# Kernel tuning notes

Hardware: AMD Instinct MI355X
Metric: run time of the kernel (lower is better)

Reference implementation:

```python
import jax, jax.numpy as jnp
import numpy as np

N = 100000      # nodes
E = 600000      # edges
IN = 128        # in_dim
HID = 32        # hidden_dim per head (layer 1)
HEADS = 4       # num_heads (layer 1)
NEG_SLOPE = 0.2 # PyG GATConv default negative_slope


def setup_inputs() -> dict:
    key = jax.random.key(0)
    ks = jax.random.split(key, 10)
    x = jax.random.normal(ks[0], (N, IN), dtype=jnp.float32)
    edge_index = jax.random.randint(ks[1], (2, E), 0, N, dtype=jnp.int64)
    # layer 1 params: W1 [IN, HEADS*HID], attention vectors [HEADS, HID], bias [HEADS*HID]
    W1 = jax.random.normal(ks[2], (IN, HEADS * HID), dtype=jnp.float32) / np.float32(np.sqrt(IN))
    att_src1 = jax.random.normal(ks[3], (HEADS, HID), dtype=jnp.float32) * 0.1
    att_dst1 = jax.random.normal(ks[4], (HEADS, HID), dtype=jnp.float32) * 0.1
    b1 = jnp.zeros((HEADS * HID,), dtype=jnp.float32)
    # layer 2 params: heads=1, out channels=1, concat=False
    W2 = jax.random.normal(ks[5], (HEADS * HID, 1), dtype=jnp.float32) / np.float32(np.sqrt(HEADS * HID))
    att_src2 = jax.random.normal(ks[6], (1, 1), dtype=jnp.float32) * 0.1
    att_dst2 = jax.random.normal(ks[7], (1, 1), dtype=jnp.float32) * 0.1
    b2 = jnp.zeros((1,), dtype=jnp.float32)
    return {"x": x, "edge_index": edge_index, "W1": W1, "att_src1": att_src1,
            "att_dst1": att_dst1, "b1": b1, "W2": W2, "att_src2": att_src2,
            "att_dst2": att_dst2, "b2": b2}


def gat_layer(x, src, dst, W, a_src, a_dst, b, heads, ch, concat):
    """PyG GATConv (eval mode): edge score + segment softmax + scatter aggregate."""
    n = x.shape[0]
    h = (x @ W).reshape(n, heads, ch)                    # [N,H,C]
    e_src = jnp.einsum('nhc,hc->nh', h, a_src)           # alpha_src per node
    e_dst = jnp.einsum('nhc,hc->nh', h, a_dst)           # alpha_dst per node
    e = jax.nn.leaky_relu(e_src[src] + e_dst[dst], NEG_SLOPE)  # [E,H]
    m = jax.ops.segment_max(e, dst, num_segments=n)      # stable softmax per dst
    p = jnp.exp(e - m[dst])
    denom = jax.ops.segment_sum(p, dst, num_segments=n)
    alpha = p / (denom[dst] + 1e-16)                     # [E,H]
    out = jax.ops.segment_sum(alpha[:, :, None] * h[src], dst, num_segments=n)  # [N,H,C]
    out = out.reshape(n, heads * ch) if concat else out.mean(axis=1)
    return out + b


def reference(x, edge_index, W1, att_src1, att_dst1, b1, W2, att_src2, att_dst2, b2):
    n = x.shape[0]
    loops = jnp.arange(n, dtype=edge_index.dtype)        # PyG add_self_loops=True
    src = jnp.concatenate([edge_index[0], loops])
    dst = jnp.concatenate([edge_index[1], loops])
    h1 = gat_layer(x, src, dst, W1, att_src1, att_dst1, b1, HEADS, HID, True)   # [N, HEADS*HID]
    out = gat_layer(h1, src, dst, W2, att_src2, att_dst2, b2, 1, 1, False)      # [N, 1]
    return out
```

## Files before the change

### kernel.cpp

```cpp
#include <hip/hip_runtime.h>
#include <hip/hip_fp16.h>
#include <math.h>

#define N_NODES 100000
#define E_EDGES 600000
#define IN_DIM  128
#define HID     32
#define HEADS   4
#define NEG     0.2f
#define CAP     32

typedef __attribute__((ext_vector_type(8))) _Float16 f16x8;
typedef __attribute__((ext_vector_type(4))) float f32x4;

__device__ __forceinline__ float lrelu(float v) { return v > 0.f ? v : NEG * v; }

#define SWZ(r, byteoff) ((byteoff) ^ (((r) & 7) << 4))


__global__ __launch_bounds__(128) void wprep_kernel(const float* __restrict__ W1,
                                                    const float* __restrict__ as1,
                                                    const float* __restrict__ ad1,
                                                    __half* __restrict__ wtx,
                                                    int* __restrict__ cnt) {
    int tid = blockIdx.x * 128 + threadIdx.x;
    for (int i = tid; i < N_NODES; i += 144 * 128) cnt[i] = 0;

    int b = blockIdx.x;
    int t = threadIdx.x;
    float v;
    if (b < 128) {
        v = W1[t * 128 + b];
    } else if (b < 136) {
        int h = b - 128;
        int hh = h & 3;
        const float* av = (h < 4) ? (as1 + hh * 32) : (ad1 + hh * 32);
        float s = 0.f;
        #pragma unroll 8
        for (int c = 0; c < 32; ++c) s += W1[t * 128 + hh * 32 + c] * av[c];
        v = s;
    } else {
        v = 0.f;
    }
    wtx[b * 128 + t] = __float2half(v);
}


__global__ __launch_bounds__(256) void scatter_kernel(const int* __restrict__ ei,
                                                      int* __restrict__ cnt,
                                                      int* __restrict__ idxb) {
    int e = blockIdx.x * 256 + threadIdx.x;
    if (e < E_EDGES) {
        int d = ei[E_EDGES + e];
        int slot = atomicAdd(&cnt[d], 1);
        if (slot < CAP) idxb[d * CAP + slot] = ei[e];
    }
}


__global__ __launch_bounds__(256) void gemm1_kernel(const float* __restrict__ x,
                                                    const __half* __restrict__ wtx,
                                                    __half* __restrict__ h1h,
                                                    float* __restrict__ aab) {
    __shared__ __half lx[64 * 128];
    __shared__ __half lw[144 * 128];
    int t = threadIdx.x;
    int row0 = blockIdx.x * 64;

    #pragma unroll
    for (int it = 0; it < 9; ++it) {
        int idx = t + it * 256;
        int r = idx >> 4, c = idx & 15;
        uint4 v = ((const uint4*)wtx)[idx];
        *(uint4*)((char*)lw + SWZ(r, r * 256 + c * 16)) = v;
    }
    #pragma unroll
    for (int it = 0; it < 8; ++it) {
        int idx = t + it * 256;
        int r = idx >> 5, c = idx & 31;
        int gr = row0 + r;
        float4 v = make_float4(0.f, 0.f, 0.f, 0.f);
        if (gr < N_NODES) v = ((const float4*)x)[gr * 32 + c];
        union { uint2 u; __half2 h[2]; } pk;
        pk.h[0] = __floats2half2_rn(v.x, v.y);
        pk.h[1] = __floats2half2_rn(v.z, v.w);
        *(uint2*)((char*)lx + SWZ(r, r * 256 + c * 8)) = pk.u;
    }
    __syncthreads();

    int w = t >> 6, lane = t & 63;
    int li = lane & 15, g = lane >> 4;
    int arow = w * 16 + li;

    f16x8 af[4];
    #pragma unroll
    for (int kt = 0; kt < 4; ++kt)
        af[kt] = *(const f16x8*)((const char*)lx + SWZ(arow, arow * 256 + kt * 64 + g * 16));

    f32x4 acc[9];
    #pragma unroll
    for (int ct = 0; ct < 9; ++ct) acc[ct] = (f32x4){0.f, 0.f, 0.f, 0.f};

    #pragma unroll
    for (int ct = 0; ct < 9; ++ct) {
        int n = ct * 16 + li;
        #pragma unroll
        for (int kt = 0; kt < 4; ++kt) {
            f16x8 bf = *(const f16x8*)((const char*)lw + SWZ(n, n * 256 + kt * 64 + g * 16));
            acc[ct] = __builtin_amdgcn_mfma_f32_16x16x32_f16(af[kt], bf, acc[ct], 0, 0, 0);
        }
    }

    int gr0 = row0 + w * 16 + g * 4;
    #pragma unroll
    for (int ct = 0; ct < 8; ++ct) {
        int col = ct * 16 + li;
        #pragma unroll
        for (int q = 0; q < 4; ++q) {
            int gr = gr0 + q;
            if (gr < N_NODES) h1h[gr * 128 + col] = __float2half(acc[ct][q]);
        }
    }
    if (li < 8) {
        #pragma unroll
        for (int q = 0; q < 4; ++q) {
            int gr = gr0 + q;
            if (gr < N_NODES) aab[gr * 8 + li] = acc[8][q];
        }
    }
}


__global__ __launch_bounds__(256) void agg1_kernel(const __half* __restrict__ h1h,
                                                   const float* __restrict__ aab,
                                                   const int* __restrict__ cnt,
                                                   const int* __restrict__ idxb,
                                                   const float* __restrict__ b1,
                                                   const float* __restrict__ W2,
                                                   const float* __restrict__ att_src2,
                                                   const float* __restrict__ att_dst2,
                                                   float* __restrict__ h2,
                                                   float* __restrict__ a2s,
                                                   float* __restrict__ a2d) {
    int lane = threadIdx.x & 63;
    int n = blockIdx.x * 4 + (threadIdx.x >> 6);
    int half = lane >> 5;
    int c4 = lane & 31;
    int h = c4 >> 3;
    int deg = min(cnt[n], CAP);
    const int* nb = idxb + n * CAP;
    float adn = aab[n * 8 + 4 + h];

    float acc0 = 0.f, acc1 = 0.f, acc2 = 0.f, acc3 = 0.f, den = 0.f;

    for (int i = 0; i < deg; i += 4) {
        int e0 = i + half, e1 = i + 2 + half;
        bool v0 = e0 < deg, v1 = e1 < deg;
        int s0 = v0 ? nb[e0] : n;
        int s1 = v1 ? nb[e1] : n;
        float a0 = aab[s0 * 8 + h];
        float a1 = aab[s1 * 8 + h];
        union { uint2 u; __half2 hh[2]; } u0, u1;
        u0.u = *(const uint2*)&h1h[s0 * 128 + c4 * 4];
        u1.u = *(const uint2*)&h1h[s1 * 128 + c4 * 4];
        float p0 = v0 ? __expf(lrelu(a0 + adn)) : 0.f;
        float p1 = v1 ? __expf(lrelu(a1 + adn)) : 0.f;
        float2 f00 = __half22float2(u0.hh[0]), f01 = __half22float2(u0.hh[1]);
        float2 f10 = __half22float2(u1.hh[0]), f11 = __half22float2(u1.hh[1]);
        acc0 += p0 * f00.x + p1 * f10.x;
        acc1 += p0 * f00.y + p1 * f10.y;
        acc2 += p0 * f01.x + p1 * f11.x;
        acc3 += p0 * f01.y + p1 * f11.y;
        den  += p0 + p1;
    }

    acc0 += __shfl_xor(acc0, 32, 64);
    acc1 += __shfl_xor(acc1, 32, 64);
    acc2 += __shfl_xor(acc2, 32, 64);
    acc3 += __shfl_xor(acc3, 32, 64);
    den  += __shfl_xor(den, 32, 64);

    {
        float p = __expf(lrelu(aab[n * 8 + h] + adn));
        union { uint2 u; __half2 hh[2]; } u;
        u.u = *(const uint2*)&h1h[n * 128 + c4 * 4];
        float2 f0 = __half22float2(u.hh[0]), f1 = __half22float2(u.hh[1]);
        acc0 += p * f0.x; acc1 += p * f0.y;
        acc2 += p * f1.x; acc3 += p * f1.y;
        den += p;
    }

    float inv = 1.f / (den + 1e-16f);
    float4 bv = ((const float4*)b1)[c4];
    float o0 = acc0 * inv + bv.x;
    float o1 = acc1 * inv + bv.y;
    float o2 = acc2 * inv + bv.z;
    float o3 = acc3 * inv + bv.w;

    float4 wv = ((const float4*)W2)[c4];
    float pp = o0 * wv.x + o1 * wv.y + o2 * wv.z + o3 * wv.w;
    #pragma unroll
    for (int m = 1; m <= 16; m <<= 1) pp += __shfl_xor(pp, m, 64);
    if (lane == 0) {
        h2[n] = pp;
        a2s[n] = pp * att_src2[0];
        a2d[n] = pp * att_dst2[0];
    }
}


__global__ __launch_bounds__(256) void agg2_kernel(const float* __restrict__ h2,
                                                   const float* __restrict__ a2s,
                                                   const float* __restrict__ a2d,
                                                   const int* __restrict__ cnt,
                                                   const int* __restrict__ idxb,
                                                   const float* __restrict__ b2,
                                                   float* __restrict__ out) {
    int n = blockIdx.x * 256 + threadIdx.x;
    if (n >= N_NODES) return;
    float adn = a2d[n];
    int deg = min(cnt[n], CAP);
    const int* nb = idxb + n * CAP;
    float num = 0.f, den = 0.f;
    for (int i = 0; i < deg; i += 4) {
        int s[4]; bool val[4]; float as_[4], hs[4];
        #pragma unroll
        for (int j = 0; j < 4; ++j) {
            val[j] = (i + j) < deg;
            s[j] = val[j] ? nb[i + j] : n;
        }
        #pragma unroll
        for (int j = 0; j < 4; ++j) as_[j] = a2s[s[j]];
        #pragma unroll
        for (int j = 0; j < 4; ++j) hs[j] = h2[s[j]];
        #pragma unroll
        for (int j = 0; j < 4; ++j) {
            float p = val[j] ? __expf(lrelu(as_[j] + adn)) : 0.f;
            num += p * hs[j];
            den += p;
        }
    }
    {
        float p = __expf(lrelu(a2s[n] + adn));
        num += p * h2[n];
        den += p;
    }
    out[n] = num / (den + 1e-16f) + b2[0];
}


extern "C" void kernel_launch(void* const* d_in, const int* in_sizes, int n_in,
                              void* d_out, int out_size, void* d_ws, size_t ws_size,
                              hipStream_t stream) {
    const float* x        = (const float*)d_in[0];
    const int*   ei       = (const int*)d_in[1];
    const float* W1       = (const float*)d_in[2];
    const float* att_src1 = (const float*)d_in[3];
    const float* att_dst1 = (const float*)d_in[4];
    const float* b1       = (const float*)d_in[5];
    const float* W2       = (const float*)d_in[6];
    const float* att_src2 = (const float*)d_in[7];
    const float* att_dst2 = (const float*)d_in[8];
    const float* b2       = (const float*)d_in[9];
    float* out = (float*)d_out;

    char* ws = (char*)d_ws;
    size_t off = 0;
    auto alloc = [&](size_t bytes) {
        char* p = ws + off;
        off = (off + bytes + 255) & ~(size_t)255;
        return p;
    };
    __half* h1h    = (__half*)alloc((size_t)N_NODES * 128 * 2);
    float*  aab    = (float*)alloc((size_t)N_NODES * 8 * 4);
    __half* wtx    = (__half*)alloc((size_t)144 * 128 * 2);
    float*  h2     = (float*)alloc((size_t)N_NODES * 4);
    float*  a2s    = (float*)alloc((size_t)N_NODES * 4);
    float*  a2d    = (float*)alloc((size_t)N_NODES * 4);
    int*    cnt    = (int*)alloc((size_t)N_NODES * 4);
    int*    idxb   = (int*)alloc((size_t)N_NODES * CAP * 4);

    const int NB_NODE = (N_NODES + 255) / 256;
    const int NB_EDGE = (E_EDGES + 255) / 256;
    const int NB_WAVE = (N_NODES + 3) / 4;
    const int NB_GEMM = (N_NODES + 63) / 64;

    wprep_kernel<<<144, 128, 0, stream>>>(W1, att_src1, att_dst1, wtx, cnt);
    scatter_kernel<<<NB_EDGE, 256, 0, stream>>>(ei, cnt, idxb);
    gemm1_kernel<<<NB_GEMM, 256, 0, stream>>>(x, wtx, h1h, aab);
    agg1_kernel<<<NB_WAVE, 256, 0, stream>>>(h1h, aab, cnt, idxb,
                                             b1, W2, att_src2, att_dst2,
                                             h2, a2s, a2d);
    agg2_kernel<<<NB_NODE, 256, 0, stream>>>(h2, a2s, a2d, cnt, idxb, b2, out);
}
```

Baseline: 207.5 us.

## Precompute per-edge attention weights in scatter and use fp16 accumulation in agg1

Moves the scatter kernel after the GEMM so it can compute each edge's four per-head exp scores and store them in a 16-byte record next to the source index. agg1 then reads these precomputed weights instead of gathering per-source attention values. It processes 4 edges per iteration with 16 lanes each loading 8 halfs, and accumulates in fp16 with hfma2. This cuts the gathers and exp work in the aggregation loop, but the edge buffer grows fourfold, the exp terms are not max-subtracted before the fp16 store, and fp16 accumulation costs accuracy. agg2 now reads a 16-byte record just to get the index.

```diff
diff --git a/kernel.cpp b/kernel.cpp
--- a/kernel.cpp
+++ b/kernel.cpp
@@ -46,18 +46,6 @@
 }
 
 
-__global__ __launch_bounds__(256) void scatter_kernel(const int* __restrict__ ei,
-                                                      int* __restrict__ cnt,
-                                                      int* __restrict__ idxb) {
-    int e = blockIdx.x * 256 + threadIdx.x;
-    if (e < E_EDGES) {
-        int d = ei[E_EDGES + e];
-        int slot = atomicAdd(&cnt[d], 1);
-        if (slot < CAP) idxb[d * CAP + slot] = ei[e];
-    }
-}
-
-
 __global__ __launch_bounds__(256) void gemm1_kernel(const float* __restrict__ x,
                                                     const __half* __restrict__ wtx,
                                                     __half* __restrict__ h1h,
@@ -131,10 +119,35 @@
 }
 
 
+__global__ __launch_bounds__(256) void scatter_kernel(const int* __restrict__ ei,
+                                                      const float* __restrict__ aab,
+                                                      int* __restrict__ cnt,
+                                                      uint4* __restrict__ edges) {
+    int e = blockIdx.x * 256 + threadIdx.x;
+    if (e >= E_EDGES) return;
+    int s = ei[e];
+    int d = ei[E_EDGES + e];
+    int slot = atomicAdd(&cnt[d], 1);
+    if (slot >= CAP) return;
+    float4 asv = *(const float4*)&aab[s * 8];
+    float4 adv = *(const float4*)&aab[d * 8 + 4];
+    float p0 = __expf(lrelu(asv.x + adv.x));
+    float p1 = __expf(lrelu(asv.y + adv.y));
+    float p2 = __expf(lrelu(asv.z + adv.z));
+    float p3 = __expf(lrelu(asv.w + adv.w));
+    union { __half2 h; unsigned u; } a, b;
+    a.h = __floats2half2_rn(p0, p1);
+    b.h = __floats2half2_rn(p2, p3);
+    uint4 rec;
+    rec.x = (unsigned)s; rec.y = a.u; rec.z = b.u; rec.w = 0;
+    edges[d * CAP + slot] = rec;
+}
+
+
 __global__ __launch_bounds__(256) void agg1_kernel(const __half* __restrict__ h1h,
                                                    const float* __restrict__ aab,
                                                    const int* __restrict__ cnt,
-                                                   const int* __restrict__ idxb,
+                                                   const uint4* __restrict__ edges,
                                                    const float* __restrict__ b1,
                                                    const float* __restrict__ W2,
                                                    const float* __restrict__ att_src2,
@@ -144,63 +157,78 @@
                                                    float* __restrict__ a2d) {
     int lane = threadIdx.x & 63;
     int n = blockIdx.x * 4 + (threadIdx.x >> 6);
-    int half = lane >> 5;
-    int c4 = lane & 31;
-    int h = c4 >> 3;
+    int g = lane >> 4;
+    int c = lane & 15;
+    int head = c >> 2;
     int deg = min(cnt[n], CAP);
-    const int* nb = idxb + n * CAP;
-    float adn = aab[n * 8 + 4 + h];
-
-    float acc0 = 0.f, acc1 = 0.f, acc2 = 0.f, acc3 = 0.f, den = 0.f;
+    const uint4* eb = edges + n * CAP;
+
+    __half2 acc01 = __half2(0.f, 0.f), acc23 = acc01, acc45 = acc01, acc67 = acc01;
+    float den = 0.f;
 
     for (int i = 0; i < deg; i += 4) {
-        int e0 = i + half, e1 = i + 2 + half;
-        bool v0 = e0 < deg, v1 = e1 < deg;
-        int s0 = v0 ? nb[e0] : n;
-        int s1 = v1 ? nb[e1] : n;
-        float a0 = aab[s0 * 8 + h];
-        float a1 = aab[s1 * 8 + h];
-        union { uint2 u; __half2 hh[2]; } u0, u1;
-        u0.u = *(const uint2*)&h1h[s0 * 128 + c4 * 4];
-        u1.u = *(const uint2*)&h1h[s1 * 128 + c4 * 4];
-        float p0 = v0 ? __expf(lrelu(a0 + adn)) : 0.f;
-        float p1 = v1 ? __expf(lrelu(a1 + adn)) : 0.f;
-        float2 f00 = __half22float2(u0.hh[0]), f01 = __half22float2(u0.hh[1]);
-        float2 f10 = __half22float2(u1.hh[0]), f11 = __half22float2(u1.hh[1]);
-        acc0 += p0 * f00.x + p1 * f10.x;
-        acc1 += p0 * f00.y + p1 * f10.y;
-        acc2 += p0 * f01.x + p1 * f11.x;
-        acc3 += p0 * f01.y + p1 * f11.y;
-        den  += p0 + p1;
-    }
-
-    acc0 += __shfl_xor(acc0, 32, 64);
-    acc1 += __shfl_xor(acc1, 32, 64);
-    acc2 += __shfl_xor(acc2, 32, 64);
-    acc3 += __shfl_xor(acc3, 32, 64);
-    den  += __shfl_xor(den, 32, 64);
+        int e = i + g;
+        bool valid = e < deg;
+        uint4 rec = eb[valid ? e : 0];
+        int s = valid ? (int)rec.x : n;
+        union { unsigned u; __half2 h; } py;
+        py.u = (head & 2) ? rec.z : rec.y;
+        __half ph = (head & 1) ? __high2half(py.h) : __low2half(py.h);
+        if (!valid) ph = __half(0.f);
+        __half2 pp = __half2half2(ph);
+        union { uint4 u; __half2 h[4]; } hv;
+        hv.u = *(const uint4*)&h1h[s * 128 + c * 8];
+        acc01 = __hfma2(pp, hv.h[0], acc01);
+        acc23 = __hfma2(pp, hv.h[1], acc23);
+        acc45 = __hfma2(pp, hv.h[2], acc45);
+        acc67 = __hfma2(pp, hv.h[3], acc67);
+        den += __half2float(ph);
+    }
+
+    union { unsigned u; __half2 h; } t0, t1, t2, t3;
+    #pragma unroll
+    for (int m = 16; m <= 32; m <<= 1) {
+        t0.u = __shfl_xor(*(unsigned*)&acc01, m, 64);
+        t1.u = __shfl_xor(*(unsigned*)&acc23, m, 64);
+        t2.u = __shfl_xor(*(unsigned*)&acc45, m, 64);
+        t3.u = __shfl_xor(*(unsigned*)&acc67, m, 64);
+        acc01 = __hadd2(acc01, t0.h);
+        acc23 = __hadd2(acc23, t1.h);
+        acc45 = __hadd2(acc45, t2.h);
+        acc67 = __hadd2(acc67, t3.h);
+        den += __shfl_xor(den, m, 64);
+    }
+
+    float s0 = __low2float(acc01), s1 = __high2float(acc01);
+    float s2 = __low2float(acc23), s3 = __high2float(acc23);
+    float s4 = __low2float(acc45), s5 = __high2float(acc45);
+    float s6 = __low2float(acc67), s7 = __high2float(acc67);
 
     {
-        float p = __expf(lrelu(aab[n * 8 + h] + adn));
-        union { uint2 u; __half2 hh[2]; } u;
-        u.u = *(const uint2*)&h1h[n * 128 + c4 * 4];
-        float2 f0 = __half22float2(u.hh[0]), f1 = __half22float2(u.hh[1]);
-        acc0 += p * f0.x; acc1 += p * f0.y;
-        acc2 += p * f1.x; acc3 += p * f1.y;
+        float p = __expf(lrelu(aab[n * 8 + head] + aab[n * 8 + 4 + head]));
+        union { uint4 u; __half2 h[4]; } hv;
+        hv.u = *(const uint4*)&h1h[n * 128 + c * 8];
+        float2 f0 = __half22float2(hv.h[0]), f1 = __half22float2(hv.h[1]);
+        float2 f2 = __half22float2(hv.h[2]), f3 = __half22float2(hv.h[3]);
+        s0 += p * f0.x; s1 += p * f0.y; s2 += p * f1.x; s3 += p * f1.y;
+        s4 += p * f2.x; s5 += p * f2.y; s6 += p * f3.x; s7 += p * f3.y;
         den += p;
     }
 
     float inv = 1.f / (den + 1e-16f);
-    float4 bv = ((const float4*)b1)[c4];
-    float o0 = acc0 * inv + bv.x;
-    float o1 = acc1 * inv + bv.y;
-    float o2 = acc2 * inv + bv.z;
-    float o3 = acc3 * inv + bv.w;
-
-    float4 wv = ((const float4*)W2)[c4];
-    float pp = o0 * wv.x + o1 * wv.y + o2 * wv.z + o3 * wv.w;
-    #pragma unroll
-    for (int m = 1; m <= 16; m <<= 1) pp += __shfl_xor(pp, m, 64);
+    float4 bv0 = ((const float4*)b1)[c * 2];
+    float4 bv1 = ((const float4*)b1)[c * 2 + 1];
+    float o0 = s0 * inv + bv0.x, o1 = s1 * inv + bv0.y;
+    float o2 = s2 * inv + bv0.z, o3 = s3 * inv + bv0.w;
+    float o4 = s4 * inv + bv1.x, o5 = s5 * inv + bv1.y;
+    float o6 = s6 * inv + bv1.z, o7 = s7 * inv + bv1.w;
+
+    float4 wv0 = ((const float4*)W2)[c * 2];
+    float4 wv1 = ((const float4*)W2)[c * 2 + 1];
+    float pp = o0 * wv0.x + o1 * wv0.y + o2 * wv0.z + o3 * wv0.w
+             + o4 * wv1.x + o5 * wv1.y + o6 * wv1.z + o7 * wv1.w;
+    #pragma unroll
+    for (int m = 1; m <= 8; m <<= 1) pp += __shfl_xor(pp, m, 64);
     if (lane == 0) {
         h2[n] = pp;
         a2s[n] = pp * att_src2[0];
@@ -213,21 +241,21 @@
                                                    const float* __restrict__ a2s,
                                                    const float* __restrict__ a2d,
                                                    const int* __restrict__ cnt,
-                                                   const int* __restrict__ idxb,
+                                                   const uint4* __restrict__ edges,
                                                    const float* __restrict__ b2,
                                                    float* __restrict__ out) {
     int n = blockIdx.x * 256 + threadIdx.x;
     if (n >= N_NODES) return;
     float adn = a2d[n];
     int deg = min(cnt[n], CAP);
-    const int* nb = idxb + n * CAP;
+    const uint4* eb = edges + n * CAP;
     float num = 0.f, den = 0.f;
     for (int i = 0; i < deg; i += 4) {
         int s[4]; bool val[4]; float as_[4], hs[4];
         #pragma unroll
         for (int j = 0; j < 4; ++j) {
             val[j] = (i + j) < deg;
-            s[j] = val[j] ? nb[i + j] : n;
+            s[j] = val[j] ? (int)eb[i + j].x : n;
         }
         #pragma unroll
         for (int j = 0; j < 4; ++j) as_[j] = a2s[s[j]];
@@ -278,7 +306,7 @@
     float*  a2s    = (float*)alloc((size_t)N_NODES * 4);
     float*  a2d    = (float*)alloc((size_t)N_NODES * 4);
     int*    cnt    = (int*)alloc((size_t)N_NODES * 4);
-    int*    idxb   = (int*)alloc((size_t)N_NODES * CAP * 4);
+    uint4*  edges  = (uint4*)alloc((size_t)N_NODES * CAP * 16);
 
     const int NB_NODE = (N_NODES + 255) / 256;
     const int NB_EDGE = (E_EDGES + 255) / 256;
@@ -286,10 +314,10 @@
     const int NB_GEMM = (N_NODES + 63) / 64;
 
     wprep_kernel<<<144, 128, 0, stream>>>(W1, att_src1, att_dst1, wtx, cnt);
-    scatter_kernel<<<NB_EDGE, 256, 0, stream>>>(ei, cnt, idxb);
     gemm1_kernel<<<NB_GEMM, 256, 0, stream>>>(x, wtx, h1h, aab);
-    agg1_kernel<<<NB_WAVE, 256, 0, stream>>>(h1h, aab, cnt, idxb,
+    scatter_kernel<<<NB_EDGE, 256, 0, stream>>>(ei, aab, cnt, edges);
+    agg1_kernel<<<NB_WAVE, 256, 0, stream>>>(h1h, aab, cnt, edges,
                                              b1, W2, att_src2, att_dst2,
                                              h2, a2s, a2d);
-    agg2_kernel<<<NB_NODE, 256, 0, stream>>>(h2, a2s, a2d, cnt, idxb, b2, out);
-}
+    agg2_kernel<<<NB_NODE, 256, 0, stream>>>(h2, a2s, a2d, cnt, edges, b2, out);
+}
```

After: 211.2 us. Within noise of the previous version (+1.8%).
